# Performance work log

Measured on AMD Instinct MI355X. Metric: run time of the kernel, lower is better.

The kernel has to match this reference:

```python
import jax, jax.numpy as jnp
import numpy as np

CUTN = 32
CUT_SIZE = 224
CUT_POW = 1.0


def _adaptive_avg_pool2d(crop, out_size):
    """Faithful torch F.adaptive_avg_pool2d for a square NCHW crop (static size).
    Uses a summed-area table so each output pixel averages the exact torch bin
    [floor(i*S/out), ceil((i+1)*S/out))."""
    S = crop.shape[2]
    idx = np.arange(out_size)
    s = (idx * S) // out_size                       # bin starts
    e = ((idx + 1) * S + out_size - 1) // out_size  # bin ends (ceil)
    # summed-area table, padded so P[..., i, j] = sum over crop[..., :i, :j]
    P = jnp.pad(jnp.cumsum(jnp.cumsum(crop, axis=2), axis=3),
                ((0, 0), (0, 0), (1, 0), (1, 0)))
    A = (P[:, :, e][:, :, :, e] - P[:, :, s][:, :, :, e]
         - P[:, :, e][:, :, :, s] + P[:, :, s][:, :, :, s])
    cnt = (e - s).astype(np.float32)
    return A / jnp.asarray(np.outer(cnt, cnt), crop.dtype)


def setup_inputs() -> dict:
    key = jax.random.key(0)
    B, C, H, W = 8, 3, 512, 512
    x = jax.random.normal(key, (B, C, H, W), dtype=jnp.float32)
    # Replicate torch's host-side RNG with a fixed numpy generator so sizes and
    # offsets are deterministic constants (in-range by construction).
    rng = np.random.default_rng(0)
    max_size = min(H, W)
    min_size = min(H, W, CUT_SIZE)
    sizes, oy, ox = [], [], []
    for _ in range(CUTN):
        sz = int(rng.random() ** CUT_POW * (max_size - min_size) + min_size)
        sizes.append(sz)
        oy.append(int(rng.integers(0, H - sz + 1)))
        ox.append(int(rng.integers(0, W - sz + 1)))
    return {
        "x": x,
        "sizes": jnp.asarray(sizes, jnp.int32),
        "offsets_y": jnp.asarray(oy, jnp.int32),
        "offsets_x": jnp.asarray(ox, jnp.int32),
        "cut_size": CUT_SIZE,
    }


def reference(x, sizes, offsets_y, offsets_x, cut_size):
    B, C, _, _ = x.shape
    sizes_np = np.asarray(sizes)
    oy_np = np.asarray(offsets_y)
    ox_np = np.asarray(offsets_x)
    cutouts = []
    for i in range(sizes_np.shape[0]):  # loop over fixed cutn (structural)
        sz = int(sizes_np[i])
        crop = jax.lax.dynamic_slice(
            x, (0, 0, int(oy_np[i]), int(ox_np[i])), (B, C, sz, sz))
        cutouts.append(_adaptive_avg_pool2d(crop, cut_size))
    return jnp.concatenate(cutouts, axis=0)  # [cutn*B, C, cut_size, cut_size]
```

## Files before the change

### kernel.cpp

```cpp
#include <hip/hip_runtime.h>


typedef float f32x4 __attribute__((ext_vector_type(4)));

constexpr int OUTSZ = 224;
constexpr int BB    = 8;
constexpr int CC    = 3;
constexpr int HH    = 512;
constexpr int WW    = 512;
constexpr int CUTN  = 32;

constexpr int TP     = 8;
constexpr int NBAND  = OUTSZ / TP;
constexpr int TILEF  = TP * WW + 8;
constexpr int NPLANE = BB * CC;
constexpr int NBLOCKS = NPLANE * CUTN;
constexpr int NXCD   = 8;
constexpr int CHUNK  = NBLOCKS / NXCD;

__device__ __forceinline__ void stage_issue(const float* __restrict__ plane_p,
                                            int S, int p0, int wv, int vo,
                                            f32x4 (&v)[4][4])
{
#pragma unroll
    for (int j = 0; j < 4; ++j) {
        int k  = (wv >> 1) + 2 * j;
        int p  = p0 + k;
        int rs = (p * S) / OUTSZ;
        int wp = ((p + 1) * S + OUTSZ - 1) / OUTSZ - rs;
        const f32x4* rp = (const f32x4*)(plane_p + (size_t)rs * WW);
        v[j][0] = rp[vo];
        if (wp > 1) v[j][1] = rp[vo + 128];
        if (wp > 2) v[j][2] = rp[vo + 256];
        if (wp > 3) v[j][3] = rp[vo + 384];
    }
}

__device__ __forceinline__ void stage_write(float* __restrict__ buf,
                                            int S, int p0, int wv, int vo,
                                            f32x4 (&v)[4][4])
{
    f32x4* t4 = (f32x4*)buf;
#pragma unroll
    for (int j = 0; j < 4; ++j) {
        int k  = (wv >> 1) + 2 * j;
        int p  = p0 + k;
        int rs = (p * S) / OUTSZ;
        int wp = ((p + 1) * S + OUTSZ - 1) / OUTSZ - rs;
        f32x4 a = v[j][0];
        if (wp > 1) a += v[j][1];
        if (wp > 2) a += v[j][2];
        if (wp > 3) a += v[j][3];
        float iv = (wp == 1) ? 1.0f : (wp == 2) ? 0.5f
                 : (wp == 3) ? (1.0f / 3.0f) : 0.25f;
        a *= iv;
        t4[k * 128 + vo] = a;
    }
}

template <int WIN>
__device__ __forceinline__ void pool_band(const float* __restrict__ buf,
                                          float* __restrict__ outp,
                                          int base, const float* __restrict__ w)
{
#pragma unroll
    for (int k = 0; k < TP; ++k) {
        const float* tr = buf + k * WW + base;
        float s = tr[0] * w[0];
        s = fmaf(tr[1], w[1], s);
        s = fmaf(tr[2], w[2], s);
        if (WIN == 4) s = fmaf(tr[3], w[3], s);
        outp[(size_t)k * OUTSZ] = s;
    }
}

__device__ __forceinline__ void band_barrier()
{
    asm volatile("s_waitcnt lgkmcnt(0)" ::: "memory");
    __builtin_amdgcn_s_barrier();
}

template <int WIN>
__device__ __forceinline__ void run_bands(const float* __restrict__ plane_p,
                                          float (*tile)[TILEF],
                                          float* __restrict__ outp,
                                          int S, int wv, int vo, int tid,
                                          int base, const float* __restrict__ wt,
                                          f32x4 (&v)[4][4])
{
    for (int k = 0; k < NBAND; ++k) {
        if (k + 1 < NBAND)
            stage_write(tile[(k + 1) & 1], S, (k + 1) * TP, wv, vo, v);
        if (k + 2 < NBAND)
            stage_issue(plane_p, S, (k + 2) * TP, wv, vo, v);
        if (tid < OUTSZ)
            pool_band<WIN>(tile[k & 1], outp + (size_t)k * TP * OUTSZ, base, wt);
        band_barrier();
    }
}

__global__ __launch_bounds__(256, 3) void make_cutouts_kernel(
    const float* __restrict__ x,
    const int*   __restrict__ sizes,
    const int*   __restrict__ offy,
    const int*   __restrict__ offx,
    float*       __restrict__ out)
{
    __shared__ float tile[2][TILEF];

    int gid = blockIdx.x;
    int w   = (gid % NXCD) * CHUNK + gid / NXCD;
    int plane = w / CUTN;
    int i     = w - plane * CUTN;
    int b     = plane / CC;
    int c     = plane - b * CC;

    int S  = sizes[i];
    int y0 = offy[i];
    int x0 = offx[i];
    int tid = threadIdx.x;

    const float* plane_p = x + (size_t)(plane * HH + y0) * WW;

    if (tid < 8) {
        tile[0][TP * WW + tid] = 0.0f;
        tile[1][TP * WW + tid] = 0.0f;
    }

    int wv   = __builtin_amdgcn_readfirstlane(tid >> 6);
    int lane = tid & 63;
    int vo   = ((wv & 1) << 6) + lane;

    int sq = (tid * S) / OUTSZ;
    int wq = ((tid + 1) * S + OUTSZ - 1) / OUTSZ - sq;
    float invq = (wq == 1) ? 1.0f : (wq == 2) ? 0.5f
               : (wq == 3) ? (1.0f / 3.0f) : 0.25f;
    float wt[4];
    wt[0] = invq;
    wt[1] = (wq > 1) ? invq : 0.0f;
    wt[2] = (wq > 2) ? invq : 0.0f;
    wt[3] = (wq > 3) ? invq : 0.0f;
    int base = x0 + sq;
    float* outp = out + ((size_t)((i * BB + b) * CC + c) * OUTSZ) * OUTSZ + tid;

    f32x4 v[4][4];
    stage_issue(plane_p, S, 0, wv, vo, v);
    stage_write(tile[0], S, 0, wv, vo, v);
    stage_issue(plane_p, S, TP, wv, vo, v);
    band_barrier();

    if (S <= 2 * OUTSZ)
        run_bands<3>(plane_p, tile, outp, S, wv, vo, tid, base, wt, v);
    else
        run_bands<4>(plane_p, tile, outp, S, wv, vo, tid, base, wt, v);
}

extern "C" void kernel_launch(void* const* d_in, const int* in_sizes, int n_in,
                              void* d_out, int out_size, void* d_ws, size_t ws_size,
                              hipStream_t stream) {
    const float* x     = (const float*)d_in[0];
    const int*   sizes = (const int*)d_in[1];
    const int*   offy  = (const int*)d_in[2];
    const int*   offx  = (const int*)d_in[3];
    float* out = (float*)d_out;

    make_cutouts_kernel<<<NBLOCKS, 256, 0, stream>>>(x, sizes, offy, offx, out);
}
```

Baseline: 220.3 us.

## Split each cutout plane into row chunks with smaller bands and higher occupancy

Each block now handles a quarter of the output rows (14 bands of 4 rows) instead of a full plane of 28 bands of 8 rows, which quadruples the grid. The band height shrinks, so shared-memory tiles and register staging arrays halve, and launch bounds are raised to 8 blocks per CU. Output stores become nontemporal. The aim is more latency hiding through more resident waves and better load balance across cutouts of different sizes, at the cost of more barriers per useful row and repeated per-block setup.

```diff
diff --git a/kernel.cpp b/kernel.cpp
--- a/kernel.cpp
+++ b/kernel.cpp
@@ -10,20 +10,21 @@
 constexpr int WW    = 512;
 constexpr int CUTN  = 32;
 
-constexpr int TP     = 8;
-constexpr int NBAND  = OUTSZ / TP;
+constexpr int TP     = 4;
+constexpr int BPB    = 14;
+constexpr int NCHUNK = 4;
 constexpr int TILEF  = TP * WW + 8;
 constexpr int NPLANE = BB * CC;
-constexpr int NBLOCKS = NPLANE * CUTN;
+constexpr int NBLOCKS = NPLANE * CUTN * NCHUNK;
 constexpr int NXCD   = 8;
-constexpr int CHUNK  = NBLOCKS / NXCD;
+constexpr int CHUNKSZ = NBLOCKS / NXCD;
 
 __device__ __forceinline__ void stage_issue(const float* __restrict__ plane_p,
                                             int S, int p0, int wv, int vo,
-                                            f32x4 (&v)[4][4])
+                                            f32x4 (&v)[2][4])
 {
 #pragma unroll
-    for (int j = 0; j < 4; ++j) {
+    for (int j = 0; j < 2; ++j) {
         int k  = (wv >> 1) + 2 * j;
         int p  = p0 + k;
         int rs = (p * S) / OUTSZ;
@@ -38,11 +39,11 @@
 
 __device__ __forceinline__ void stage_write(float* __restrict__ buf,
                                             int S, int p0, int wv, int vo,
-                                            f32x4 (&v)[4][4])
+                                            f32x4 (&v)[2][4])
 {
     f32x4* t4 = (f32x4*)buf;
 #pragma unroll
-    for (int j = 0; j < 4; ++j) {
+    for (int j = 0; j < 2; ++j) {
         int k  = (wv >> 1) + 2 * j;
         int p  = p0 + k;
         int rs = (p * S) / OUTSZ;
@@ -70,7 +71,7 @@
         s = fmaf(tr[1], w[1], s);
         s = fmaf(tr[2], w[2], s);
         if (WIN == 4) s = fmaf(tr[3], w[3], s);
-        outp[(size_t)k * OUTSZ] = s;
+        __builtin_nontemporal_store(s, &outp[(size_t)k * OUTSZ]);
     }
 }
 
@@ -84,22 +85,23 @@
 __device__ __forceinline__ void run_bands(const float* __restrict__ plane_p,
                                           float (*tile)[TILEF],
                                           float* __restrict__ outp,
-                                          int S, int wv, int vo, int tid,
-                                          int base, const float* __restrict__ wt,
-                                          f32x4 (&v)[4][4])
+                                          int S, int pbase, int wv, int vo,
+                                          int tid, int base,
+                                          const float* __restrict__ wt,
+                                          f32x4 (&v)[2][4])
 {
-    for (int k = 0; k < NBAND; ++k) {
-        if (k + 1 < NBAND)
-            stage_write(tile[(k + 1) & 1], S, (k + 1) * TP, wv, vo, v);
-        if (k + 2 < NBAND)
-            stage_issue(plane_p, S, (k + 2) * TP, wv, vo, v);
+    for (int k = 0; k < BPB; ++k) {
+        if (k + 1 < BPB)
+            stage_write(tile[(k + 1) & 1], S, pbase + (k + 1) * TP, wv, vo, v);
+        if (k + 2 < BPB)
+            stage_issue(plane_p, S, pbase + (k + 2) * TP, wv, vo, v);
         if (tid < OUTSZ)
             pool_band<WIN>(tile[k & 1], outp + (size_t)k * TP * OUTSZ, base, wt);
         band_barrier();
     }
 }
 
-__global__ __launch_bounds__(256, 3) void make_cutouts_kernel(
+__global__ __launch_bounds__(256, 8) void make_cutouts_kernel(
     const float* __restrict__ x,
     const int*   __restrict__ sizes,
     const int*   __restrict__ offy,
@@ -109,9 +111,11 @@
     __shared__ float tile[2][TILEF];
 
     int gid = blockIdx.x;
-    int w   = (gid % NXCD) * CHUNK + gid / NXCD;
-    int plane = w / CUTN;
-    int i     = w - plane * CUTN;
+    int w   = (gid % NXCD) * CHUNKSZ + gid / NXCD;
+    int plane = w / (CUTN * NCHUNK);
+    int rest  = w - plane * (CUTN * NCHUNK);
+    int i     = rest / NCHUNK;
+    int ch    = rest - i * NCHUNK;
     int b     = plane / CC;
     int c     = plane - b * CC;
 
@@ -119,6 +123,7 @@
     int y0 = offy[i];
     int x0 = offx[i];
     int tid = threadIdx.x;
+    int pbase = ch * (BPB * TP);
 
     const float* plane_p = x + (size_t)(plane * HH + y0) * WW;
 
@@ -141,18 +146,19 @@
     wt[2] = (wq > 2) ? invq : 0.0f;
     wt[3] = (wq > 3) ? invq : 0.0f;
     int base = x0 + sq;
-    float* outp = out + ((size_t)((i * BB + b) * CC + c) * OUTSZ) * OUTSZ + tid;
+    float* outp = out
+        + ((size_t)((i * BB + b) * CC + c) * OUTSZ + pbase) * OUTSZ + tid;
 
-    f32x4 v[4][4];
-    stage_issue(plane_p, S, 0, wv, vo, v);
-    stage_write(tile[0], S, 0, wv, vo, v);
-    stage_issue(plane_p, S, TP, wv, vo, v);
+    f32x4 v[2][4];
+    stage_issue(plane_p, S, pbase, wv, vo, v);
+    stage_write(tile[0], S, pbase, wv, vo, v);
+    stage_issue(plane_p, S, pbase + TP, wv, vo, v);
     band_barrier();
 
     if (S <= 2 * OUTSZ)
-        run_bands<3>(plane_p, tile, outp, S, wv, vo, tid, base, wt, v);
+        run_bands<3>(plane_p, tile, outp, S, pbase, wv, vo, tid, base, wt, v);
     else
-        run_bands<4>(plane_p, tile, outp, S, wv, vo, tid, base, wt, v);
+        run_bands<4>(plane_p, tile, outp, S, pbase, wv, vo, tid, base, wt, v);
 }
 
 extern "C" void kernel_launch(void* const* d_in, const int* in_sizes, int n_in,
```

New measurement: 237.3 us. 1.08x slower.
